# Performance work log

Measured on AMD Instinct MI355X. Metric: run time of the kernel, lower is better.

The kernel has to match this reference:

```python
import jax, jax.numpy as jnp
import numpy as np

K = 3
STRIDE = 1
PAD = 1


def conv2d(x, w, b, stride, pad):
    y = jax.lax.conv_general_dilated(
        x, w, (stride, stride), [(pad, pad), (pad, pad)],
        dimension_numbers=("NCHW", "OIHW", "NCHW"))
    return y + b[None, :, None, None]


def setup_inputs() -> dict:
    key = jax.random.key(0)
    k1, k2, k3, k4, k5, k6 = jax.random.split(key, 6)
    B, C, H, W = 8, 128, 64, 64
    O = 128
    x = jax.random.normal(k1, (B, C, H, W), dtype=jnp.float32)
    # torch zero-inits offset/mask convs; use small random weights so the
    # deformable sampling path is actually exercised (offsets ~O(0.5) px).
    w_offset = jax.random.normal(k2, (2 * K * K, C, K, K), dtype=jnp.float32) * 0.02
    b_offset = jax.random.normal(k3, (2 * K * K,), dtype=jnp.float32) * 0.1
    w_mask = jax.random.normal(k4, (K * K, C, K, K), dtype=jnp.float32) * 0.02
    b_mask = jax.random.normal(k5, (K * K,), dtype=jnp.float32) * 0.1
    fan_in = C * K * K
    bound = 1.0 / np.sqrt(fan_in)  # kaiming_uniform(a=sqrt(5)) bound
    weight = jax.random.uniform(k6, (O, C, K, K), dtype=jnp.float32,
                                minval=-bound, maxval=bound)
    return {"x": x, "w_offset": w_offset, "b_offset": b_offset,
            "w_mask": w_mask, "b_mask": b_mask, "weight": weight}


def deform_conv2d(x, offset, mask, weight):
    B, C, H, W = x.shape
    O = weight.shape[0]
    K2 = K * K
    Ho = (H + 2 * PAD - K) // STRIDE + 1
    Wo = (W + 2 * PAD - K) // STRIDE + 1
    # offset layout: [B, 2*K2, Ho, Wo], per-tap (dy, dx) pairs
    off = offset.reshape(B, K2, 2, Ho, Wo)
    dy, dx = off[:, :, 0], off[:, :, 1]  # [B,K2,Ho,Wo]
    ky, kx = jnp.meshgrid(jnp.arange(K), jnp.arange(K), indexing="ij")
    ky = ky.reshape(K2).astype(jnp.float32)
    kx = kx.reshape(K2).astype(jnp.float32)
    base_y = ky[:, None] + (jnp.arange(Ho, dtype=jnp.float32) * STRIDE - PAD)[None, :]  # [K2,Ho]
    base_x = kx[:, None] + (jnp.arange(Wo, dtype=jnp.float32) * STRIDE - PAD)[None, :]  # [K2,Wo]
    py = dy + base_y[None, :, :, None]  # [B,K2,Ho,Wo]
    px = dx + base_x[None, :, None, :]

    y0 = jnp.floor(py)
    x0 = jnp.floor(px)
    ly = py - y0
    lx = px - x0
    y0i = y0.astype(jnp.int32)
    x0i = x0.astype(jnp.int32)

    xf = x.reshape(B, C, H * W)
    N = K2 * Ho * Wo

    def gather(yi, xi):
        valid = (yi >= 0) & (yi < H) & (xi >= 0) & (xi < W)
        idx = jnp.clip(yi, 0, H - 1) * W + jnp.clip(xi, 0, W - 1)
        v = jnp.take_along_axis(xf, idx.reshape(B, 1, N), axis=2)  # [B,C,N]
        return v * valid.reshape(B, 1, N)

    w00 = ((1 - ly) * (1 - lx)).reshape(B, 1, N)
    w01 = ((1 - ly) * lx).reshape(B, 1, N)
    w10 = (ly * (1 - lx)).reshape(B, 1, N)
    w11 = (ly * lx).reshape(B, 1, N)
    val = (w00 * gather(y0i, x0i) + w01 * gather(y0i, x0i + 1)
           + w10 * gather(y0i + 1, x0i) + w11 * gather(y0i + 1, x0i + 1))  # [B,C,N]
    val = val.reshape(B, C, K2, Ho * Wo) * mask.reshape(B, 1, K2, Ho * Wo)
    out = jnp.einsum("oik,bikn->bon", weight.reshape(O, C, K2), val)
    return out.reshape(B, O, Ho, Wo)


def reference(x, w_offset, b_offset, w_mask, b_mask, weight):
    offset = conv2d(x, w_offset, b_offset, STRIDE, PAD)
    mask = jax.nn.sigmoid(conv2d(x, w_mask, b_mask, STRIDE, PAD))
    return deform_conv2d(x, offset, mask, weight)
```

## Files before the change

### kernel.cpp

```cpp
#include <hip/hip_runtime.h>
#include <hip/hip_fp16.h>
#include <cstdint>

#define B_    8
#define C_    128
#define HW    4096
#define O_    128
#define KDIM  1152

typedef short bf16x8 __attribute__((ext_vector_type(8)));
typedef float f32x4  __attribute__((ext_vector_type(4)));

__device__ __forceinline__ unsigned short f2bf(float f) {
  unsigned u = __float_as_uint(f);
  u += 0x7FFFu + ((u >> 16) & 1u);
  return (unsigned short)(u >> 16);
}
__device__ __forceinline__ float bf_lo(unsigned u) { return __uint_as_float(u << 16); }
__device__ __forceinline__ float bf_hi(unsigned u) { return __uint_as_float(u & 0xFFFF0000u); }

#define WS_WBF   0
#define WS_WCB   294912
#define WS_ZERO  368640
#define WS_XT    368896
#define WS_PW    8757504
#define WS_PA    11116800
#define WS_VALT  12296448
#define WS_COUT  WS_VALT

__global__ void k_prep(const float* __restrict__ weight,
                       const float* __restrict__ w_off, const float* __restrict__ w_msk,
                       unsigned short* __restrict__ Wbf, unsigned short* __restrict__ wcb,
                       float* __restrict__ zero) {
  int gid = blockIdx.x * 256 + threadIdx.x;
  if (gid < O_ * KDIM) {
    int o = gid / KDIM, i = gid - o * KDIM;
    int k2 = i >> 7, c = i & 127;
    Wbf[gid] = f2bf(weight[o * KDIM + c * 9 + k2]);
  }
  if (gid < 9 * 32 * 128) {
    int t = gid >> 12, rem = gid & 4095;
    int o = rem >> 7, c = rem & 127;
    float v = 0.f;
    if (o < 18) v = w_off[o * KDIM + c * 9 + t];
    else if (o < 27) v = w_msk[(o - 18) * KDIM + c * 9 + t];
    wcb[gid] = f2bf(v);
  }
  if (gid < 64) zero[gid] = 0.f;
}

__global__ __launch_bounds__(256) void k_xt(const float* __restrict__ x,
                                            unsigned short* __restrict__ xt) {
  __shared__ unsigned short tile[64][130];
  int bid = blockIdx.x;
  int b = bid >> 6, p0 = (bid & 63) << 6;
  int tid = threadIdx.x;
  int pl = tid & 63, cq = tid >> 6;
  const float* xb = x + (size_t)b * C_ * HW + p0 + pl;
#pragma unroll
  for (int i = 0; i < 32; ++i) {
    int c = cq * 32 + i;
    tile[pl][c] = f2bf(xb[(size_t)c * HW]);
  }
  __syncthreads();
  int cd = tid & 63, pr = tid >> 6;
  unsigned* dst = (unsigned*)xt + ((size_t)b * HW + p0) * 64 + cd;
  const unsigned* t32 = (const unsigned*)&tile[0][0];
#pragma unroll
  for (int j = 0; j < 16; ++j) {
    int p = pr + j * 4;
    dst[(size_t)p * 64] = t32[p * 65 + cd];
  }
}

__global__ __launch_bounds__(256) void k_cgemm(const unsigned short* __restrict__ xt,
                                               const unsigned short* __restrict__ wcb,
                                               const float* __restrict__ zero,
                                               float* __restrict__ cout) {
  __shared__ __align__(16) unsigned short As[2][128 * 128];
  __shared__ __align__(16) unsigned short Bs[2][32 * 128];

  int bid = blockIdx.x;
  int b = bid >> 5;
  int p0 = (bid & 31) << 7;
  int tid = threadIdx.x, lane = tid & 63, wv = tid >> 6;
  int lhi = lane >> 4, llo = lane & 15;

  const unsigned short* xb = xt + (size_t)b * HW * C_;

  auto STAGE = [&](int t, int bufi) {
    int ky = t / 3, kx = t - ky * 3;
    int dshift = (ky - 1) * 64 + (kx - 1);
#pragma unroll
    for (int i = 0; i < 8; ++i) {
      int chunk = i * 256 + tid;
      int r = chunk >> 4, j = chunk & 15;
      int p = p0 + r;
      int ho = p >> 6, wo = p & 63;
      int iy = ho + ky - 1, ix = wo + kx - 1;
      bool valid = ((unsigned)iy < 64u) && ((unsigned)ix < 64u);
      int jj = j ^ (r & 15);
      const unsigned short* src = valid ? (xb + (size_t)(p + dshift) * C_ + jj * 8)
                                        : (const unsigned short*)zero;
      __builtin_amdgcn_global_load_lds(
          (const __attribute__((address_space(1))) unsigned*)src,
          (__attribute__((address_space(3))) unsigned*)((char*)&As[bufi][0] + i * 4096 + wv * 1024),
          16, 0, 0);
    }
#pragma unroll
    for (int i = 0; i < 2; ++i) {
      int chunk = i * 256 + tid;
      int o = chunk >> 4, j = chunk & 15;
      int jj = j ^ (o & 15);
      __builtin_amdgcn_global_load_lds(
          (const __attribute__((address_space(1))) unsigned*)(wcb + (size_t)t * 4096 + o * 128 + jj * 8),
          (__attribute__((address_space(3))) unsigned*)((char*)&Bs[bufi][0] + i * 4096 + wv * 1024),
          16, 0, 0);
    }
  };

  f32x4 acc[2][2] = {};
  STAGE(0, 0);
  __syncthreads();
  int buf = 0;
  for (int t = 0; t < 9; ++t) {
    if (t < 8) STAGE(t + 1, buf ^ 1);
    bf16x8 bfv[2][4];
#pragma unroll
    for (int n = 0; n < 2; ++n)
#pragma unroll
      for (int ks = 0; ks < 4; ++ks) {
        int row = n * 16 + llo;
        int off = row * 256 + (((ks * 4 + lhi) ^ (row & 15)) << 4);
        bfv[n][ks] = *(const bf16x8*)((const char*)&Bs[buf][0] + off);
      }
#pragma unroll
    for (int ks = 0; ks < 4; ++ks) {
      bf16x8 af[2];
#pragma unroll
      for (int m = 0; m < 2; ++m) {
        int row = wv * 32 + m * 16 + llo;
        int off = row * 256 + (((ks * 4 + lhi) ^ (row & 15)) << 4);
        af[m] = *(const bf16x8*)((const char*)&As[buf][0] + off);
      }
#pragma unroll
      for (int m = 0; m < 2; ++m)
#pragma unroll
        for (int n = 0; n < 2; ++n)
          acc[m][n] = __builtin_amdgcn_mfma_f32_16x16x32_bf16(af[m], bfv[n][ks], acc[m][n], 0, 0, 0);
    }
    __syncthreads();
    buf ^= 1;
  }

  float* cb = cout + ((size_t)b * HW + p0) * 32;
#pragma unroll
  for (int m = 0; m < 2; ++m)
#pragma unroll
    for (int n = 0; n < 2; ++n)
#pragma unroll
      for (int r = 0; r < 4; ++r) {
        int pix = wv * 32 + m * 16 + lhi * 4 + r;
        int o = n * 16 + llo;
        cb[(size_t)pix * 32 + o] = acc[m][n][r];
      }
}

__global__ __launch_bounds__(256) void k_rp(const float* __restrict__ cout,
                                            const float* __restrict__ b_off,
                                            const float* __restrict__ b_msk,
                                            uint2* __restrict__ pwh,
                                            unsigned* __restrict__ paw) {
  int gid = blockIdx.x * 256 + threadIdx.x;
  int b = gid >> 12, p = gid & 4095;
  const float* cr = cout + (size_t)gid * 32;
  float v[28];
#pragma unroll
  for (int j = 0; j < 7; ++j) *(f32x4*)&v[j * 4] = *(const f32x4*)(cr + j * 4);
  int ho = p >> 6, wo = p & 63;
#pragma unroll
  for (int k2 = 0; k2 < 9; ++k2) {
    int ky = k2 / 3, kx = k2 - ky * 3;
    float dy = v[2 * k2] + b_off[2 * k2];
    float dx = v[2 * k2 + 1] + b_off[2 * k2 + 1];
    float mk = v[18 + k2] + b_msk[k2];
    mk = 1.f / (1.f + __expf(-mk));
    float py = dy + (float)(ho + ky - 1);
    float px = dx + (float)(wo + kx - 1);
    float fy = floorf(py), fx = floorf(px);
    float ly = py - fy, lx = px - fx;
    int y0 = (int)fy, x0 = (int)fx;
    float vy0 = ((unsigned)y0 < 64u) ? 1.f : 0.f;
    float vy1 = ((unsigned)(y0 + 1) < 64u) ? 1.f : 0.f;
    float vx0 = ((unsigned)x0 < 64u) ? 1.f : 0.f;
    float vx1 = ((unsigned)(x0 + 1) < 64u) ? 1.f : 0.f;
    int cy0 = min(max(y0, 0), 63);
    int cx0 = min(max(x0, 0), 63);
    float wy0 = (1.f - ly) * mk, wy1 = ly * mk;
    float w00 = wy0 * (1.f - lx) * vy0 * vx0, w01 = wy0 * lx * vy0 * vx1;
    float w10 = wy1 * (1.f - lx) * vy1 * vx0, w11 = wy1 * lx * vy1 * vx1;
    int dxf = (x0 >= 0 && x0 <= 62) ? 1 : 0;
    int dyf = (y0 >= 0 && y0 <= 62) ? 1 : 0;
    unsigned h00 = __half_as_ushort(__float2half_rn(w00));
    unsigned h01 = __half_as_ushort(__float2half_rn(w01));
    unsigned h10 = __half_as_ushort(__float2half_rn(w10));
    unsigned h11 = __half_as_ushort(__float2half_rn(w11));
    int idx = (b * 9 + k2) * HW + p;
    pwh[idx] = make_uint2(h00 | (h01 << 16), h10 | (h11 << 16));
    paw[idx] = (unsigned)(cy0 * 64 + cx0) | (dxf << 12) | (dyf << 13);
  }
}

__global__ __launch_bounds__(256) void k_sample(const unsigned* __restrict__ xt32,
                                                const uint2* __restrict__ pwh,
                                                const unsigned* __restrict__ paw,
                                                unsigned* __restrict__ valT32) {
  int tid = threadIdx.x;
  int lane = tid & 63;
  int wuni = __builtin_amdgcn_readfirstlane(tid >> 6);
  int task = blockIdx.x * 4 + wuni;
  int k2 = task % 9;
  int bp = task / 9;
  int b = bp >> 12, p = bp & 4095;
  int pidx = (b * 9 + k2) * HW + p;

  uint2 W = pwh[pidx];
  unsigned aw = paw[pidx];
  __half2 h0 = *reinterpret_cast<__half2*>(&W.x);
  __half2 h1 = *reinterpret_cast<__half2*>(&W.y);
  float2 f0 = __half22float2(h0), f1 = __half22float2(h1);
  float w00 = f0.x, w01 = f0.y, w10 = f1.x, w11 = f1.y;

  unsigned a00 = (aw & 4095u) << 6;
  unsigned dxs = ((aw >> 12) & 1u) << 6;
  unsigned dys = ((aw >> 13) & 1u) << 12;

  const unsigned* xb = xt32 + ((size_t)b << 18);
  unsigned v00 = xb[a00 + lane];
  unsigned v01 = xb[a00 + dxs + lane];
  unsigned v10 = xb[a00 + dys + lane];
  unsigned v11 = xb[a00 + dys + dxs + lane];

  float lo = w00 * bf_lo(v00) + w01 * bf_lo(v01) + w10 * bf_lo(v10) + w11 * bf_lo(v11);
  float hi = w00 * bf_hi(v00) + w01 * bf_hi(v01) + w10 * bf_hi(v10) + w11 * bf_hi(v11);
  unsigned pk = (unsigned)f2bf(lo) | ((unsigned)f2bf(hi) << 16);
  valT32[(size_t)bp * 576 + k2 * 64 + lane] = pk;
}

__global__ __launch_bounds__(256, 2) void k_gemm(const unsigned short* __restrict__ Wbf,
                                                 const unsigned short* __restrict__ valT,
                                                 float* __restrict__ out) {
  __shared__ __align__(16) unsigned short As[2][128 * 64];
  __shared__ __align__(16) unsigned short Bs[2][64 * 64];

  int bid = blockIdx.x;
  int b = bid >> 6;
  int pbase = (bid & 63) << 6;
  int tid = threadIdx.x, lane = tid & 63, wv = tid >> 6;
  int lhi = lane >> 4, llo = lane & 15;

  const unsigned short* vb = valT + ((size_t)b * HW + pbase) * KDIM;

  f32x4 acc[2][4] = {};

  auto STAGE = [&](int kt, int bufi) {
#pragma unroll
    for (int j = 0; j < 4; ++j) {
      int chunk = j * 256 + tid;
      int row = chunk >> 3;
      int sch = (chunk & 7) ^ (row & 7);
      __builtin_amdgcn_global_load_lds(
          (const __attribute__((address_space(1))) unsigned*)(Wbf + (size_t)row * KDIM + kt * 64 + sch * 8),
          (__attribute__((address_space(3))) unsigned*)((char*)&As[bufi][0] + j * 4096 + wv * 1024),
          16, 0, 0);
    }
#pragma unroll
    for (int j = 0; j < 2; ++j) {
      int chunk = j * 256 + tid;
      int row = chunk >> 3;
      int sch = (chunk & 7) ^ (row & 7);
      __builtin_amdgcn_global_load_lds(
          (const __attribute__((address_space(1))) unsigned*)(vb + (size_t)row * KDIM + kt * 64 + sch * 8),
          (__attribute__((address_space(3))) unsigned*)((char*)&Bs[bufi][0] + j * 4096 + wv * 1024),
          16, 0, 0);
    }
  };

  STAGE(0, 0);
  __syncthreads();

  int buf = 0;
  for (int kt = 0; kt < 18; ++kt) {
    if (kt < 17) STAGE(kt + 1, buf ^ 1);
#pragma unroll
    for (int ks = 0; ks < 2; ++ks) {
      bf16x8 af[2], bfv[4];
#pragma unroll
      for (int m = 0; m < 2; ++m) {
        int row = wv * 32 + m * 16 + llo;
        int off = row * 128 + ((ks * 64 + lhi * 16) ^ ((llo & 7) << 4));
        af[m] = *(const bf16x8*)((const char*)&As[buf][0] + off);
      }
#pragma unroll
      for (int n = 0; n < 4; ++n) {
        int row = n * 16 + llo;
        int off = row * 128 + ((ks * 64 + lhi * 16) ^ ((llo & 7) << 4));
        bfv[n] = *(const bf16x8*)((const char*)&Bs[buf][0] + off);
      }
#pragma unroll
      for (int m = 0; m < 2; ++m)
#pragma unroll
        for (int n = 0; n < 4; ++n)
          acc[m][n] = __builtin_amdgcn_mfma_f32_16x16x32_bf16(af[m], bfv[n], acc[m][n], 0, 0, 0);
    }
    __syncthreads();
    buf ^= 1;
  }

  float* ob = out + (size_t)b * O_ * HW + pbase;
#pragma unroll
  for (int m = 0; m < 2; ++m) {
    int o0 = wv * 32 + m * 16 + lhi * 4;
#pragma unroll
    for (int n = 0; n < 4; ++n) {
      int pl = n * 16 + llo;
#pragma unroll
      for (int r = 0; r < 4; ++r)
        ob[(size_t)(o0 + r) * HW + pl] = acc[m][n][r];
    }
  }
}

extern "C" void kernel_launch(void* const* d_in, const int* in_sizes, int n_in,
                              void* d_out, int out_size, void* d_ws, size_t ws_size,
                              hipStream_t stream) {
  const float* x      = (const float*)d_in[0];
  const float* w_off  = (const float*)d_in[1];
  const float* b_off  = (const float*)d_in[2];
  const float* w_msk  = (const float*)d_in[3];
  const float* b_msk  = (const float*)d_in[4];
  const float* weight = (const float*)d_in[5];
  float* out = (float*)d_out;
  char* ws = (char*)d_ws;

  unsigned short* Wbf  = (unsigned short*)(ws + WS_WBF);
  unsigned short* wcb  = (unsigned short*)(ws + WS_WCB);
  float*          zero = (float*)(ws + WS_ZERO);
  unsigned short* xt   = (unsigned short*)(ws + WS_XT);
  uint2*          pwh  = (uint2*)(ws + WS_PW);
  unsigned*       paw  = (unsigned*)(ws + WS_PA);
  float*          cgo  = (float*)(ws + WS_COUT);
  unsigned short* valT = (unsigned short*)(ws + WS_VALT);

  k_prep  <<<576, 256, 0, stream>>>(weight, w_off, w_msk, Wbf, wcb, zero);
  k_xt    <<<512, 256, 0, stream>>>(x, xt);
  k_cgemm <<<256, 256, 0, stream>>>(xt, wcb, zero, cgo);
  k_rp    <<<128, 256, 0, stream>>>(cgo, b_off, b_msk, pwh, paw);
  k_sample<<<73728, 256, 0, stream>>>((const unsigned*)xt, pwh, paw, (unsigned*)valT);
  k_gemm  <<<512, 256, 0, stream>>>(Wbf, valT, out);
}
```

Measured before the change: 155.8 us.

## Fuse bilinear sampling into GEMM, building B tiles directly in shared memory

```diff
diff --git a/kernel.cpp b/kernel.cpp
--- a/kernel.cpp
+++ b/kernel.cpp
@@ -25,8 +25,7 @@
 #define WS_XT    368896
 #define WS_PW    8757504
 #define WS_PA    11116800
-#define WS_VALT  12296448
-#define WS_COUT  WS_VALT
+#define WS_COUT  12296448
 
 __global__ void k_prep(const float* __restrict__ weight,
                        const float* __restrict__ w_off, const float* __restrict__ w_msk,
@@ -211,59 +210,58 @@
   }
 }
 
-__global__ __launch_bounds__(256) void k_sample(const unsigned* __restrict__ xt32,
-                                                const uint2* __restrict__ pwh,
-                                                const unsigned* __restrict__ paw,
-                                                unsigned* __restrict__ valT32) {
-  int tid = threadIdx.x;
-  int lane = tid & 63;
-  int wuni = __builtin_amdgcn_readfirstlane(tid >> 6);
-  int task = blockIdx.x * 4 + wuni;
-  int k2 = task % 9;
-  int bp = task / 9;
-  int b = bp >> 12, p = bp & 4095;
-  int pidx = (b * 9 + k2) * HW + p;
-
-  uint2 W = pwh[pidx];
-  unsigned aw = paw[pidx];
-  __half2 h0 = *reinterpret_cast<__half2*>(&W.x);
-  __half2 h1 = *reinterpret_cast<__half2*>(&W.y);
-  float2 f0 = __half22float2(h0), f1 = __half22float2(h1);
-  float w00 = f0.x, w01 = f0.y, w10 = f1.x, w11 = f1.y;
-
-  unsigned a00 = (aw & 4095u) << 6;
-  unsigned dxs = ((aw >> 12) & 1u) << 6;
-  unsigned dys = ((aw >> 13) & 1u) << 12;
-
-  const unsigned* xb = xt32 + ((size_t)b << 18);
-  unsigned v00 = xb[a00 + lane];
-  unsigned v01 = xb[a00 + dxs + lane];
-  unsigned v10 = xb[a00 + dys + lane];
-  unsigned v11 = xb[a00 + dys + dxs + lane];
-
-  float lo = w00 * bf_lo(v00) + w01 * bf_lo(v01) + w10 * bf_lo(v10) + w11 * bf_lo(v11);
-  float hi = w00 * bf_hi(v00) + w01 * bf_hi(v01) + w10 * bf_hi(v10) + w11 * bf_hi(v11);
-  unsigned pk = (unsigned)f2bf(lo) | ((unsigned)f2bf(hi) << 16);
-  valT32[(size_t)bp * 576 + k2 * 64 + lane] = pk;
-}
-
-__global__ __launch_bounds__(256, 2) void k_gemm(const unsigned short* __restrict__ Wbf,
-                                                 const unsigned short* __restrict__ valT,
-                                                 float* __restrict__ out) {
+__global__ __launch_bounds__(256) void k_fused(const unsigned* __restrict__ xt32,
+                                               const uint2* __restrict__ pwh,
+                                               const unsigned* __restrict__ paw,
+                                               const unsigned short* __restrict__ Wbf,
+                                               float* __restrict__ out) {
   __shared__ __align__(16) unsigned short As[2][128 * 64];
-  __shared__ __align__(16) unsigned short Bs[2][64 * 64];
+  __shared__ __align__(16) unsigned short Bs[2][64 * 128];
 
   int bid = blockIdx.x;
   int b = bid >> 6;
   int pbase = (bid & 63) << 6;
-  int tid = threadIdx.x, lane = tid & 63, wv = tid >> 6;
+  int tid = threadIdx.x, lane = tid & 63;
+  int wuni = __builtin_amdgcn_readfirstlane(tid >> 6);
+  int wr = wuni >> 1, wc = wuni & 1;
   int lhi = lane >> 4, llo = lane & 15;
 
-  const unsigned short* vb = valT + ((size_t)b * HW + pbase) * KDIM;
-
-  f32x4 acc[2][4] = {};
-
-  auto STAGE = [&](int kt, int bufi) {
+  const unsigned* xb32 = xt32 + ((size_t)b << 18);
+
+  uint2 Wv[8]; unsigned awv[8]; unsigned g[32];
+
+  auto B_ISSUE = [&](int k2n, int half) {
+    int pp0 = wuni * 16 + half * 8;
+    int pidx0 = (b * 9 + k2n) * HW + pbase + pp0;
+#pragma unroll
+    for (int i = 0; i < 8; ++i) { Wv[i] = pwh[pidx0 + i]; awv[i] = paw[pidx0 + i]; }
+#pragma unroll
+    for (int i = 0; i < 8; ++i) {
+      unsigned aw = awv[i];
+      unsigned a00 = (aw & 4095u) << 6;
+      unsigned dxs = ((aw >> 12) & 1u) << 6;
+      unsigned dys = ((aw >> 13) & 1u) << 12;
+      g[i * 4 + 0] = xb32[a00 + lane];
+      g[i * 4 + 1] = xb32[a00 + dxs + lane];
+      g[i * 4 + 2] = xb32[a00 + dys + lane];
+      g[i * 4 + 3] = xb32[a00 + dys + dxs + lane];
+    }
+  };
+  auto B_FIN = [&](int bufn, int half) {
+#pragma unroll
+    for (int i = 0; i < 8; ++i) {
+      float2 f0 = __half22float2(*reinterpret_cast<__half2*>(&Wv[i].x));
+      float2 f1 = __half22float2(*reinterpret_cast<__half2*>(&Wv[i].y));
+      unsigned v00 = g[i*4], v01 = g[i*4+1], v10 = g[i*4+2], v11 = g[i*4+3];
+      float lo = f0.x*bf_lo(v00) + f0.y*bf_lo(v01) + f1.x*bf_lo(v10) + f1.y*bf_lo(v11);
+      float hi = f0.x*bf_hi(v00) + f0.y*bf_hi(v01) + f1.x*bf_hi(v10) + f1.y*bf_hi(v11);
+      unsigned pk = (unsigned)f2bf(lo) | ((unsigned)f2bf(hi) << 16);
+      int row = wuni * 16 + half * 8 + i;
+      unsigned off = (unsigned)(row * 256) + (((unsigned)lane * 4u) ^ ((unsigned)(row & 7) << 4));
+      *(unsigned*)((char*)&Bs[bufn][0] + off) = pk;
+    }
+  };
+  auto STAGE_A = [&](int kt, int abuf) {
 #pragma unroll
     for (int j = 0; j < 4; ++j) {
       int chunk = j * 256 + tid;
@@ -271,62 +269,65 @@
       int sch = (chunk & 7) ^ (row & 7);
       __builtin_amdgcn_global_load_lds(
           (const __attribute__((address_space(1))) unsigned*)(Wbf + (size_t)row * KDIM + kt * 64 + sch * 8),
-          (__attribute__((address_space(3))) unsigned*)((char*)&As[bufi][0] + j * 4096 + wv * 1024),
+          (__attribute__((address_space(3))) unsigned*)((char*)&As[abuf][0] + j * 4096 + wuni * 1024),
           16, 0, 0);
     }
-#pragma unroll
-    for (int j = 0; j < 2; ++j) {
-      int chunk = j * 256 + tid;
-      int row = chunk >> 3;
-      int sch = (chunk & 7) ^ (row & 7);
-      __builtin_amdgcn_global_load_lds(
-          (const __attribute__((address_space(1))) unsigned*)(vb + (size_t)row * KDIM + kt * 64 + sch * 8),
-          (__attribute__((address_space(3))) unsigned*)((char*)&Bs[bufi][0] + j * 4096 + wv * 1024),
-          16, 0, 0);
-    }
-  };
-
-  STAGE(0, 0);
+  };
+
+  f32x4 acc[4][2] = {};
+  auto MSTEP = [&](int abuf, int bbuf, int bhalf) {
+#pragma unroll
+    for (int ks = 0; ks < 2; ++ks) {
+      bf16x8 af[4], bfv[2];
+#pragma unroll
+      for (int m = 0; m < 4; ++m) {
+        int row = wr * 64 + m * 16 + llo;
+        int off = row * 128 + ((ks * 64 + lhi * 16) ^ ((llo & 7) << 4));
+        af[m] = *(const bf16x8*)((const char*)&As[abuf][0] + off);
+      }
+#pragma unroll
+      for (int n = 0; n < 2; ++n) {
+        int row = wc * 32 + n * 16 + llo;
+        int off = row * 256 + ((bhalf * 128 + ks * 64 + lhi * 16) ^ ((row & 7) << 4));
+        bfv[n] = *(const bf16x8*)((const char*)&Bs[bbuf][0] + off);
+      }
+#pragma unroll
+      for (int m = 0; m < 4; ++m)
+#pragma unroll
+        for (int n = 0; n < 2; ++n)
+          acc[m][n] = __builtin_amdgcn_mfma_f32_16x16x32_bf16(af[m], bfv[n], acc[m][n], 0, 0, 0);
+    }
+  };
+
+  B_ISSUE(0, 0); B_FIN(0, 0);
+  B_ISSUE(0, 1); B_FIN(0, 1);
+  STAGE_A(0, 0);
   __syncthreads();
 
-  int buf = 0;
-  for (int kt = 0; kt < 18; ++kt) {
-    if (kt < 17) STAGE(kt + 1, buf ^ 1);
-#pragma unroll
-    for (int ks = 0; ks < 2; ++ks) {
-      bf16x8 af[2], bfv[4];
-#pragma unroll
-      for (int m = 0; m < 2; ++m) {
-        int row = wv * 32 + m * 16 + llo;
-        int off = row * 128 + ((ks * 64 + lhi * 16) ^ ((llo & 7) << 4));
-        af[m] = *(const bf16x8*)((const char*)&As[buf][0] + off);
-      }
-#pragma unroll
-      for (int n = 0; n < 4; ++n) {
-        int row = n * 16 + llo;
-        int off = row * 128 + ((ks * 64 + lhi * 16) ^ ((llo & 7) << 4));
-        bfv[n] = *(const bf16x8*)((const char*)&Bs[buf][0] + off);
-      }
-#pragma unroll
-      for (int m = 0; m < 2; ++m)
-#pragma unroll
-        for (int n = 0; n < 4; ++n)
-          acc[m][n] = __builtin_amdgcn_mfma_f32_16x16x32_bf16(af[m], bfv[n], acc[m][n], 0, 0, 0);
-    }
+  for (int k2 = 0; k2 < 9; ++k2) {
+    int kt0 = 2 * k2;
+    if (kt0 + 1 < 18) STAGE_A(kt0 + 1, (kt0 + 1) & 1);
+    if (k2 < 8) B_ISSUE(k2 + 1, 0);
+    MSTEP(kt0 & 1, k2 & 1, 0);
+    if (k2 < 8) B_FIN((k2 + 1) & 1, 0);
     __syncthreads();
-    buf ^= 1;
+    if (kt0 + 2 < 18) STAGE_A(kt0 + 2, (kt0 + 2) & 1);
+    if (k2 < 8) B_ISSUE(k2 + 1, 1);
+    MSTEP((kt0 + 1) & 1, k2 & 1, 1);
+    if (k2 < 8) B_FIN((k2 + 1) & 1, 1);
+    __syncthreads();
   }
 
   float* ob = out + (size_t)b * O_ * HW + pbase;
 #pragma unroll
-  for (int m = 0; m < 2; ++m) {
-    int o0 = wv * 32 + m * 16 + lhi * 4;
-#pragma unroll
-    for (int n = 0; n < 4; ++n) {
-      int pl = n * 16 + llo;
+  for (int m = 0; m < 4; ++m) {
+    int o0 = wr * 64 + m * 16 + lhi * 4;
+#pragma unroll
+    for (int n = 0; n < 2; ++n) {
+      int px = wc * 32 + n * 16 + llo;
 #pragma unroll
       for (int r = 0; r < 4; ++r)
-        ob[(size_t)(o0 + r) * HW + pl] = acc[m][n][r];
+        ob[(size_t)(o0 + r) * HW + px] = acc[m][n][r];
     }
   }
 }
@@ -350,12 +351,10 @@
   uint2*          pwh  = (uint2*)(ws + WS_PW);
   unsigned*       paw  = (unsigned*)(ws + WS_PA);
   float*          cgo  = (float*)(ws + WS_COUT);
-  unsigned short* valT = (unsigned short*)(ws + WS_VALT);
 
   k_prep  <<<576, 256, 0, stream>>>(weight, w_off, w_msk, Wbf, wcb, zero);
   k_xt    <<<512, 256, 0, stream>>>(x, xt);
   k_cgemm <<<256, 256, 0, stream>>>(xt, wcb, zero, cgo);
   k_rp    <<<128, 256, 0, stream>>>(cgo, b_off, b_msk, pwh, paw);
-  k_sample<<<73728, 256, 0, stream>>>((const unsigned*)xt, pwh, paw, (unsigned*)valT);
-  k_gemm  <<<512, 256, 0, stream>>>(Wbf, valT, out);
-}
+  k_fused <<<512, 256, 0, stream>>>((const unsigned*)xt, pwh, paw, Wbf, out);
+}
```

Result: faster. 132.4 us (-15.0%).
